# Kernel optimization log

Hardware: AMD Instinct MI355X
Metric: run time of the kernel (lower is better)

Reference implementation:

```python
import jax, jax.numpy as jnp
import numpy as np

B, S, D, H, DH, K, M = 2, 1024, 1024, 16, 64, 32, 8192
LN_EPS = 1e-5


def _ln(x, g, b):
    mu = jnp.mean(x, axis=-1, keepdims=True)
    var = jnp.var(x, axis=-1, keepdims=True)
    return (x - mu) * jax.lax.rsqrt(var + LN_EPS) * g + b


def _split_heads(t):  # [B,S,H*DH] -> [B,H,S,DH]
    return t.reshape(B, S, H, DH).transpose(0, 2, 1, 3)


def setup_inputs() -> dict:
    key = jax.random.key(0)
    ks = jax.random.split(key, 10)
    sd = 1.0 / np.sqrt(D)
    return {
        "x": jax.random.normal(ks[0], (B, S, D), jnp.float32),
        "mem_k_db": jax.random.normal(ks[1], (B, M, D), jnp.float32),
        "mem_v_db": jax.random.normal(ks[2], (B, M, D), jnp.float32),
        "g_val": jax.random.uniform(ks[3], (H,), jnp.float32),
        "ln1_g": jnp.ones((D,), jnp.float32),
        "ln1_b": jnp.zeros((D,), jnp.float32),
        "W_attn": jax.random.normal(ks[4], (D, 3 * D), jnp.float32) * sd,
        "b_attn": jnp.zeros((3 * D,), jnp.float32),
        "W_proj": jax.random.normal(ks[5], (D, D), jnp.float32) * sd,
        "b_proj": jnp.zeros((D,), jnp.float32),
        "ln2_g": jnp.ones((D,), jnp.float32),
        "ln2_b": jnp.zeros((D,), jnp.float32),
        "W_fc": jax.random.normal(ks[6], (D, 4 * D), jnp.float32) * sd,
        "b_fc": jnp.zeros((4 * D,), jnp.float32),
        "W_out": jax.random.normal(ks[7], (4 * D, D), jnp.float32) / np.sqrt(4 * D),
        "b_out": jnp.zeros((D,), jnp.float32),
    }


def reference(x, mem_k_db, mem_v_db, g_val, ln1_g, ln1_b, W_attn, b_attn,
              W_proj, b_proj, ln2_g, ln2_b, W_fc, b_fc, W_out, b_out):
    residual = x
    h = _ln(x, ln1_g, ln1_b)
    qkv = h @ W_attn + b_attn                       # [B,S,3D]
    q_f, k_f, v_f = jnp.split(qkv, 3, axis=-1)      # each [B,S,D]
    q = _split_heads(q_f)                           # [B,H,S,DH]
    k = _split_heads(k_f)
    v = _split_heads(v_f)

    # --- kNN memory search (non-per-head path): l2-normalized concat-head query ---
    sq = q_f / jnp.linalg.norm(q_f, axis=-1, keepdims=True).clip(1e-12)
    sims = jnp.einsum('bsd,bmd->bsm', sq, mem_k_db)          # [B,S,M]
    _, idx = jax.lax.top_k(sims, K)                          # [B,S,K]
    idx_e = idx[..., None]                                   # [B,S,K,1]
    mem_k = jnp.take_along_axis(mem_k_db[:, None], idx_e, axis=2)  # [B,S,K,D]
    mem_v = jnp.take_along_axis(mem_v_db[:, None], idx_e, axis=2)  # [B,S,K,D]
    # split memory into heads: [B,S,K,H*DH] -> [B,H,S,K,DH]
    mem_k = mem_k.reshape(B, S, K, H, DH).transpose(0, 3, 1, 2, 4)
    mem_v = mem_v.reshape(B, S, K, H, DH).transpose(0, 3, 1, 2, 4)

    inv_sqrt_dh = 1.0 / np.sqrt(DH)
    mem_w = jnp.einsum('bhid,bhijd->bhij', q, mem_k) * inv_sqrt_dh   # [B,H,S,K]

    std_w = jnp.einsum('bhid,bhjd->bhij', q, k) * inv_sqrt_dh        # [B,H,S,S]
    causal = jnp.tril(jnp.ones((S, S), bool))
    mask_val = jnp.finfo(std_w.dtype).min
    std_w = jnp.where(causal, std_w, mask_val)

    all_w = jax.nn.softmax(jnp.concatenate([mem_w, std_w], axis=-1), axis=-1)
    mem_attn, local_attn = all_w[..., :K], all_w[..., K:]

    local_out = jnp.einsum('bhij,bhjd->bhid', local_attn, v)
    mem_out = jnp.einsum('bhij,bhijd->bhid', mem_attn, mem_v)

    g = g_val.reshape(1, H, 1, 1)
    attn_out = (1.0 - g) * local_out + g * mem_out           # [B,H,S,DH]
    attn_out = attn_out.transpose(0, 2, 1, 3).reshape(B, S, D)
    attn_out = attn_out @ W_proj + b_proj

    h = attn_out + residual
    residual2 = h
    h = _ln(h, ln2_g, ln2_b)
    h = jax.nn.gelu(h @ W_fc + b_fc, approximate=True) @ W_out + b_out
    return residual2 + h
```

## Files before the change

kernel.cpp:

```cpp
#include <hip/hip_runtime.h>
#include <stdint.h>

#define DEV static __device__ __forceinline__

typedef __attribute__((ext_vector_type(8))) __bf16 bf16x8;
typedef __attribute__((ext_vector_type(4))) float f32x4;

DEV float bf2f(uint32_t u) {
  union { uint32_t i; float f; } v; v.i = u << 16; return v.f;
}
DEV uint16_t f2bf(float f) {
  union { float f; uint32_t i; } v; v.f = f;
  uint32_t x = v.i;
  return (uint16_t)((x + 0x7FFFu + ((x >> 16) & 1u)) >> 16);
}
DEV f32x4 mfma16(bf16x8 a, bf16x8 b, f32x4 c) {
  return __builtin_amdgcn_mfma_f32_16x16x32_bf16(a, b, c, 0, 0, 0);
}
DEV bf16x8 as_bf16x8(uint4 u) { return __builtin_bit_cast(bf16x8, u); }

DEV void gload16(const uint16_t* __restrict__ g, uint16_t* l) {
  __builtin_amdgcn_global_load_lds(
      (const __attribute__((address_space(1))) uint32_t*)g,
      (__attribute__((address_space(3))) uint32_t*)l, 16, 0, 0);
}

DEV float gelu_tanh(float x) {
  float x3 = x * x * x;
  float u = 0.7978845608028654f * (x + 0.044715f * x3);
  return 0.5f * x * (1.0f + tanhf(u));
}
DEV unsigned mono_key(float f) {
  union { float f; uint32_t u; } v; v.f = f;
  return (v.u & 0x80000000u) ? ~v.u : (v.u | 0x80000000u);
}
DEV unsigned mono16(unsigned u) {
  return (u & 0x8000u) ? (~u & 0xFFFFu) : (u | 0x8000u);
}

__global__ __launch_bounds__(256) void k_transpose_cast(
    const float* __restrict__ in, uint16_t* __restrict__ out,
    uint16_t* __restrict__ outlo, int R, int C) {
  __shared__ float tile[32][33];
  int c0 = blockIdx.x * 32, r0 = blockIdx.y * 32;
  int tx = threadIdx.x % 32, ty = threadIdx.x / 32;
  for (int i = 0; i < 32; i += 8)
    tile[ty + i][tx] = in[(size_t)(r0 + ty + i) * C + c0 + tx];
  __syncthreads();
  for (int i = 0; i < 32; i += 8) {
    float v = tile[tx][ty + i];
    uint16_t hi = f2bf(v);
    out[(size_t)(c0 + ty + i) * R + r0 + tx] = hi;
    if (outlo)
      outlo[(size_t)(c0 + ty + i) * R + r0 + tx] = f2bf(v - bf2f(hi));
  }
}

__global__ __launch_bounds__(256) void k_cast_bf16(
    const float* __restrict__ in, uint16_t* __restrict__ out, long n) {
  long i = ((long)blockIdx.x * 256 + threadIdx.x) * 4;
  if (i >= n) return;
  float4 v = *(const float4*)(in + i);
  uint2 pk;
  pk.x = (uint32_t)f2bf(v.x) | ((uint32_t)f2bf(v.y) << 16);
  pk.y = (uint32_t)f2bf(v.z) | ((uint32_t)f2bf(v.w) << 16);
  *(uint2*)(out + i) = pk;
}

__global__ __launch_bounds__(256) void k_layernorm(
    const float* __restrict__ x, const float* __restrict__ g,
    const float* __restrict__ bb, uint16_t* __restrict__ out,
    uint16_t* __restrict__ outlo) {
  int row = blockIdx.x;
  const float* xr = x + (size_t)row * 1024;
  int c = threadIdx.x * 4;
  float4 v = *(const float4*)(xr + c);
  float s = v.x + v.y + v.z + v.w;
  float s2 = v.x * v.x + v.y * v.y + v.z * v.z + v.w * v.w;
  for (int off = 32; off; off >>= 1) {
    s += __shfl_down(s, off, 64);
    s2 += __shfl_down(s2, off, 64);
  }
  __shared__ float ps[4], qs[4];
  int lane = threadIdx.x & 63, wv = threadIdx.x >> 6;
  if (!lane) { ps[wv] = s; qs[wv] = s2; }
  __syncthreads();
  float S = ps[0] + ps[1] + ps[2] + ps[3];
  float S2 = qs[0] + qs[1] + qs[2] + qs[3];
  float mu = S * (1.f / 1024.f);
  float var = S2 * (1.f / 1024.f) - mu * mu;
  float rinv = rsqrtf(var + 1e-5f);
  const float* vv = (const float*)&v;
  uint16_t o[4], ol[4];
#pragma unroll
  for (int j = 0; j < 4; j++) {
    float y = (vv[j] - mu) * rinv * g[c + j] + bb[c + j];
    o[j] = f2bf(y);
    ol[j] = f2bf(y - bf2f(o[j]));
  }
  uint2 pk;
  pk.x = (uint32_t)o[0] | ((uint32_t)o[1] << 16);
  pk.y = (uint32_t)o[2] | ((uint32_t)o[3] << 16);
  *(uint2*)(out + (size_t)row * 1024 + c) = pk;
  if (outlo) {
    pk.x = (uint32_t)ol[0] | ((uint32_t)ol[1] << 16);
    pk.y = (uint32_t)ol[2] | ((uint32_t)ol[3] << 16);
    *(uint2*)(outlo + (size_t)row * 1024 + c) = pk;
  }
}

template <int EPI>
__global__ __launch_bounds__(256) void k_gemm2(
    const uint16_t* __restrict__ A, int lda,
    const uint16_t* __restrict__ Bt, int ldb,
    void* __restrict__ Cout, int ldc,
    const float* __restrict__ bias,
    const float* __restrict__ resid,
    int Kc) {
  const int m0 = blockIdx.y * 64, n0 = blockIdx.x * 128;
  const int kt0 = (EPI & 16) ? blockIdx.z * Kc : 0;
  __shared__ __align__(16) uint16_t As[64 * 64];
  __shared__ __align__(16) uint16_t Bs[128 * 64];
  const int t = threadIdx.x, l = t & 63, w = t >> 6;
  const int lg = l >> 4, lr = l & 15;

  const int rS = t >> 3, cS = t & 7;
  const int csS = cS ^ (rS & 7);
  const uint16_t* pa1 = A + (size_t)(m0 + rS) * lda + kt0 + csS * 8;
  const uint16_t* pa2 = pa1 + (size_t)32 * lda;
  const uint16_t* pb1 = Bt + (size_t)(n0 + rS) * ldb + kt0 + csS * 8;
  const uint16_t* pb2 = pb1 + (size_t)32 * ldb;
  const uint16_t* pb3 = pb1 + (size_t)64 * ldb;
  const uint16_t* pb4 = pb1 + (size_t)96 * ldb;
  uint16_t* la1 = As + w * 512;
  uint16_t* la2 = As + 2048 + w * 512;
  uint16_t* lb1 = Bs + w * 512;
  uint16_t* lb2 = Bs + 2048 + w * 512;
  uint16_t* lb3 = Bs + 4096 + w * 512;
  uint16_t* lb4 = Bs + 6144 + w * 512;

  int offA[2][4], offB[2][2];
#pragma unroll
  for (int kk = 0; kk < 2; kk++) {
#pragma unroll
    for (int i = 0; i < 4; i++) {
      int row = i * 16 + lr;
      offA[kk][i] = row * 64 + (((kk * 4 + lg) ^ (row & 7)) * 8);
    }
#pragma unroll
    for (int j = 0; j < 2; j++) {
      int row = w * 32 + j * 16 + lr;
      offB[kk][j] = row * 64 + (((kk * 4 + lg) ^ (row & 7)) * 8);
    }
  }

  f32x4 acc[4][2] = {};
  for (int kt = 0; kt < Kc; kt += 64) {
    __syncthreads();
    gload16(pa1, la1); gload16(pa2, la2);
    gload16(pb1, lb1); gload16(pb2, lb2);
    gload16(pb3, lb3); gload16(pb4, lb4);
    pa1 += 64; pa2 += 64; pb1 += 64; pb2 += 64; pb3 += 64; pb4 += 64;
    __syncthreads();
#pragma unroll
    for (int kk = 0; kk < 2; kk++) {
      bf16x8 af[4], bfr[2];
#pragma unroll
      for (int i = 0; i < 4; i++) af[i] = as_bf16x8(*(const uint4*)(As + offA[kk][i]));
#pragma unroll
      for (int j = 0; j < 2; j++) bfr[j] = as_bf16x8(*(const uint4*)(Bs + offB[kk][j]));
#pragma unroll
      for (int i = 0; i < 4; i++)
#pragma unroll
        for (int j = 0; j < 2; j++)
          acc[i][j] = mfma16(af[i], bfr[j], acc[i][j]);
    }
  }
  const size_t zoff = (EPI & 16) ? (size_t)blockIdx.z * gridDim.y * 64 * ldc : 0;
#pragma unroll
  for (int i = 0; i < 4; i++)
#pragma unroll
    for (int j = 0; j < 2; j++)
#pragma unroll
      for (int r = 0; r < 4; r++) {
        int row = m0 + i * 16 + lg * 4 + r;
        int col = n0 + w * 32 + j * 16 + lr;
        float v = acc[i][j][r];
        if constexpr (EPI & 16) {
          ((float*)Cout)[zoff + (size_t)row * ldc + col] = v;
        } else {
          if constexpr (EPI & 1) v += bias[col];
          if constexpr (EPI & 4) v = gelu_tanh(v);
          if constexpr (EPI & 2) v += resid[(size_t)row * ldc + col];
          if constexpr (EPI & 8)
            ((uint16_t*)Cout)[(size_t)row * ldc + col] = f2bf(v);
          else
            ((float*)Cout)[(size_t)row * ldc + col] = v;
        }
      }
}

__global__ __launch_bounds__(256) void k_gemm_sims(
    const uint16_t* __restrict__ A,
    const uint16_t* __restrict__ Bt,
    uint16_t* __restrict__ Cout) {
  const int m0 = blockIdx.y * 64, n0 = blockIdx.x * 128;
  A += (size_t)blockIdx.z * 1024 * 3072;
  Bt += (size_t)blockIdx.z * 8192 * 1024;
  __shared__ __align__(16) uint16_t As[64 * 64];
  __shared__ __align__(16) uint16_t Bs[128 * 64];
  const int t = threadIdx.x, l = t & 63, w = t >> 6;
  const int lg = l >> 4, lr = l & 15;

  const int rS = t >> 3, cS = t & 7;
  const int csS = cS ^ (rS & 7);
  const uint16_t* pa1 = A + (size_t)(m0 + rS) * 3072 + csS * 8;
  const uint16_t* pa2 = pa1 + 32 * 3072;
  const uint16_t* pb1 = Bt + (size_t)(n0 + rS) * 1024 + csS * 8;
  const uint16_t* pb2 = pb1 + 32 * 1024;
  const uint16_t* pb3 = pb1 + 64 * 1024;
  const uint16_t* pb4 = pb1 + 96 * 1024;
  uint16_t* la1 = As + w * 512;
  uint16_t* la2 = As + 2048 + w * 512;
  uint16_t* lb1 = Bs + w * 512;
  uint16_t* lb2 = Bs + 2048 + w * 512;
  uint16_t* lb3 = Bs + 4096 + w * 512;
  uint16_t* lb4 = Bs + 6144 + w * 512;

  int offA[2][4], offB[2][2];
#pragma unroll
  for (int kk = 0; kk < 2; kk++) {
#pragma unroll
    for (int i = 0; i < 4; i++) {
      int row = i * 16 + lr;
      offA[kk][i] = row * 64 + (((kk * 4 + lg) ^ (row & 7)) * 8);
    }
#pragma unroll
    for (int j = 0; j < 2; j++) {
      int row = w * 32 + j * 16 + lr;
      offB[kk][j] = row * 64 + (((kk * 4 + lg) ^ (row & 7)) * 8);
    }
  }

  f32x4 acc[4][2] = {};
  for (int kt = 0; kt < 1024; kt += 64) {
    __syncthreads();
    gload16(pa1, la1); gload16(pa2, la2);
    gload16(pb1, lb1); gload16(pb2, lb2);
    gload16(pb3, lb3); gload16(pb4, lb4);
    pa1 += 64; pa2 += 64; pb1 += 64; pb2 += 64; pb3 += 64; pb4 += 64;
    __syncthreads();
#pragma unroll
    for (int kk = 0; kk < 2; kk++) {
      bf16x8 af[4], bfr[2];
#pragma unroll
      for (int i = 0; i < 4; i++) af[i] = as_bf16x8(*(const uint4*)(As + offA[kk][i]));
#pragma unroll
      for (int j = 0; j < 2; j++) bfr[j] = as_bf16x8(*(const uint4*)(Bs + offB[kk][j]));
#pragma unroll
      for (int i = 0; i < 4; i++)
#pragma unroll
        for (int j = 0; j < 2; j++)
          acc[i][j] = mfma16(af[i], bfr[j], acc[i][j]);
    }
  }
  const size_t zoff = (size_t)blockIdx.z * 1024 * 8192;
#pragma unroll
  for (int i = 0; i < 4; i++)
#pragma unroll
    for (int j = 0; j < 2; j++)
#pragma unroll
      for (int r = 0; r < 4; r++) {
        int row = m0 + i * 16 + lg * 4 + r;
        int col = n0 + w * 32 + j * 16 + lr;
        Cout[zoff + (size_t)row * 8192 + col] = f2bf(acc[i][j][r]);
      }
}

__global__ __launch_bounds__(256) void k_gemm_split2(
    const uint16_t* __restrict__ Ah, const uint16_t* __restrict__ Al, int lda,
    const uint16_t* __restrict__ Bh, const uint16_t* __restrict__ Bl, int ldb,
    uint16_t* __restrict__ Ch, uint16_t* __restrict__ Cl, int ldc,
    const float* __restrict__ bias, int Kd) {
  const int m0 = blockIdx.y * 64, n0 = blockIdx.x * 128;
  __shared__ __align__(16) uint16_t Ahs[64 * 64];
  __shared__ __align__(16) uint16_t Als[64 * 64];
  __shared__ __align__(16) uint16_t Bhs[128 * 64];
  __shared__ __align__(16) uint16_t Bls[128 * 64];
  const int t = threadIdx.x, l = t & 63, w = t >> 6;
  const int lg = l >> 4, lr = l & 15;

  const int rS = t >> 3, cS = t & 7;
  const int csS = cS ^ (rS & 7);
  const size_t ao1 = (size_t)(m0 + rS) * lda + csS * 8;
  const size_t bo1 = (size_t)(n0 + rS) * ldb + csS * 8;
  const uint16_t* pah1 = Ah + ao1; const uint16_t* pah2 = pah1 + (size_t)32 * lda;
  const uint16_t* pal1 = Al + ao1; const uint16_t* pal2 = pal1 + (size_t)32 * lda;
  const uint16_t* pbh1 = Bh + bo1; const uint16_t* pbh2 = pbh1 + (size_t)32 * ldb;
  const uint16_t* pbh3 = pbh1 + (size_t)64 * ldb; const uint16_t* pbh4 = pbh1 + (size_t)96 * ldb;
  const uint16_t* pbl1 = Bl + bo1; const uint16_t* pbl2 = pbl1 + (size_t)32 * ldb;
  const uint16_t* pbl3 = pbl1 + (size_t)64 * ldb; const uint16_t* pbl4 = pbl1 + (size_t)96 * ldb;
  uint16_t* lah1 = Ahs + w * 512; uint16_t* lah2 = Ahs + 2048 + w * 512;
  uint16_t* lal1 = Als + w * 512; uint16_t* lal2 = Als + 2048 + w * 512;
  uint16_t* lbh1 = Bhs + w * 512; uint16_t* lbh2 = Bhs + 2048 + w * 512;
  uint16_t* lbh3 = Bhs + 4096 + w * 512; uint16_t* lbh4 = Bhs + 6144 + w * 512;
  uint16_t* lbl1 = Bls + w * 512; uint16_t* lbl2 = Bls + 2048 + w * 512;
  uint16_t* lbl3 = Bls + 4096 + w * 512; uint16_t* lbl4 = Bls + 6144 + w * 512;

  int offA[2][4], offB[2][2];
#pragma unroll
  for (int kk = 0; kk < 2; kk++) {
#pragma unroll
    for (int i = 0; i < 4; i++) {
      int row = i * 16 + lr;
      offA[kk][i] = row * 64 + (((kk * 4 + lg) ^ (row & 7)) * 8);
    }
#pragma unroll
    for (int j = 0; j < 2; j++) {
      int row = w * 32 + j * 16 + lr;
      offB[kk][j] = row * 64 + (((kk * 4 + lg) ^ (row & 7)) * 8);
    }
  }

  f32x4 acc[4][2] = {};
  for (int kt = 0; kt < Kd; kt += 64) {
    __syncthreads();
    gload16(pah1, lah1); gload16(pah2, lah2);
    gload16(pal1, lal1); gload16(pal2, lal2);
    gload16(pbh1, lbh1); gload16(pbh2, lbh2);
    gload16(pbh3, lbh3); gload16(pbh4, lbh4);
    gload16(pbl1, lbl1); gload16(pbl2, lbl2);
    gload16(pbl3, lbl3); gload16(pbl4, lbl4);
    pah1 += 64; pah2 += 64; pal1 += 64; pal2 += 64;
    pbh1 += 64; pbh2 += 64; pbh3 += 64; pbh4 += 64;
    pbl1 += 64; pbl2 += 64; pbl3 += 64; pbl4 += 64;
    __syncthreads();
#pragma unroll
    for (int kk = 0; kk < 2; kk++) {
      bf16x8 ah[4], al[4], bh[2], bl[2];
#pragma unroll
      for (int i = 0; i < 4; i++) {
        ah[i] = as_bf16x8(*(const uint4*)(Ahs + offA[kk][i]));
        al[i] = as_bf16x8(*(const uint4*)(Als + offA[kk][i]));
      }
#pragma unroll
      for (int j = 0; j < 2; j++) {
        bh[j] = as_bf16x8(*(const uint4*)(Bhs + offB[kk][j]));
        bl[j] = as_bf16x8(*(const uint4*)(Bls + offB[kk][j]));
      }
#pragma unroll
      for (int i = 0; i < 4; i++)
#pragma unroll
        for (int j = 0; j < 2; j++) {
          acc[i][j] = mfma16(ah[i], bh[j], acc[i][j]);
          acc[i][j] = mfma16(ah[i], bl[j], acc[i][j]);
          acc[i][j] = mfma16(al[i], bh[j], acc[i][j]);
        }
    }
  }
#pragma unroll
  for (int i = 0; i < 4; i++)
#pragma unroll
    for (int j = 0; j < 2; j++)
#pragma unroll
      for (int r = 0; r < 4; r++) {
        int row = m0 + i * 16 + lg * 4 + r;
        int col = n0 + w * 32 + j * 16 + lr;
        float v = acc[i][j][r] + bias[col];
        uint16_t hi = f2bf(v);
        Ch[(size_t)row * ldc + col] = hi;
        Cl[(size_t)row * ldc + col] = f2bf(v - bf2f(hi));
      }
}

template <int NP>
__global__ __launch_bounds__(256) void k_merge(
    const float* __restrict__ parts, const float* __restrict__ bias,
    const float* __restrict__ resid, float* __restrict__ out) {
  int row = blockIdx.x, c = threadIdx.x * 4;
  size_t off = (size_t)row * 1024 + c;
  float4 s = *(const float4*)(resid + off);
  float4 bv = *(const float4*)(bias + c);
  s.x += bv.x; s.y += bv.y; s.z += bv.z; s.w += bv.w;
#pragma unroll
  for (int z = 0; z < NP; z++) {
    float4 pv = *(const float4*)(parts + (size_t)z * 2048 * 1024 + off);
    s.x += pv.x; s.y += pv.y; s.z += pv.z; s.w += pv.w;
  }
  *(float4*)(out + off) = s;
}

__global__ __launch_bounds__(256) void k_topk2(
    const uint16_t* __restrict__ simsb,
    const uint16_t* __restrict__ qkvh_b,
    const uint16_t* __restrict__ qkvl_b,
    const float* __restrict__ memk_b,
    int* __restrict__ idx_out,
    float* __restrict__ mlogh) {
  int grow = blockIdx.x;
  int z = grow >> 10;
  int t = threadIdx.x;
  const uint16_t* s16 = simsb + (size_t)grow * 8192;
  const float* memk = memk_b + (size_t)z * 8192 * 1024;
  unsigned key[32];
#pragma unroll
  for (int k = 0; k < 4; k++) {
    uint4 u = *(const uint4*)(s16 + t * 8 + k * 2048);
    const uint16_t* pu = (const uint16_t*)&u;
#pragma unroll
    for (int j = 0; j < 8; j++) key[k * 8 + j] = mono16(pu[j]);
  }
  __shared__ int partial[2][4];
  __shared__ int cnt_s;
  __shared__ int sidx[40];
  __shared__ float qs[1024];
  __shared__ float hval[40][16];
  int lane = t & 63, wv = t >> 6;
  unsigned lo = 0u, hi = 0xFFFFu;
  for (int it = 0; it < 16; ++it) {
    unsigned mid = lo + ((hi - lo) >> 1);
    int c = 0;
#pragma unroll
    for (int i = 0; i < 32; i++) c += (key[i] > mid) ? 1 : 0;
    for (int off = 32; off; off >>= 1) c += __shfl_down(c, off, 64);
    if (!lane) partial[it & 1][wv] = c;
    __syncthreads();
    int tot = partial[it & 1][0] + partial[it & 1][1] +
              partial[it & 1][2] + partial[it & 1][3];
    if (tot >= 40) lo = mid + 1; else hi = mid;
  }
  unsigned T = lo;
  if (t == 0) cnt_s = 0;
  __syncthreads();
#pragma unroll
  for (int i = 0; i < 32; i++)
    if (key[i] > T) {
      int p = atomicAdd(&cnt_s, 1);
      if (p < 40) sidx[p] = t * 8 + (i >> 3) * 2048 + (i & 7);
    }
  __syncthreads();
#pragma unroll
  for (int i = 0; i < 32; i++)
    if (key[i] == T) {
      int p = atomicAdd(&cnt_s, 1);
      if (p < 40) sidx[p] = t * 8 + (i >> 3) * 2048 + (i & 7);
    }
  {
    int c4 = t * 4;
    const uint16_t* qh = qkvh_b + (size_t)grow * 3072;
    const uint16_t* ql = qkvl_b + (size_t)grow * 3072;
    uint2 uh = *(const uint2*)(qh + c4);
    uint2 ul = *(const uint2*)(ql + c4);
    qs[c4 + 0] = bf2f(uh.x & 0xFFFF) + bf2f(ul.x & 0xFFFF);
    qs[c4 + 1] = bf2f(uh.x >> 16) + bf2f(ul.x >> 16);
    qs[c4 + 2] = bf2f(uh.y & 0xFFFF) + bf2f(ul.y & 0xFFFF);
    qs[c4 + 3] = bf2f(uh.y >> 16) + bf2f(ul.y >> 16);
  }
  __syncthreads();
  {
    float4 qreg[4];
#pragma unroll
    for (int i = 0; i < 4; i++) qreg[i] = *(const float4*)(qs + i * 256 + lane * 4);
    for (int cc = 0; cc < 10; ++cc) {
      int c = wv * 10 + cc;
      const float* kp = memk + (size_t)sidx[c] * 1024;
#pragma unroll
      for (int i = 0; i < 4; ++i) {
        float4 kv = *(const float4*)(kp + i * 256 + lane * 4);
        float pband = kv.x * qreg[i].x + kv.y * qreg[i].y +
                      kv.z * qreg[i].z + kv.w * qreg[i].w;
        pband += __shfl_xor(pband, 1, 64);
        pband += __shfl_xor(pband, 2, 64);
        pband += __shfl_xor(pband, 4, 64);
        pband += __shfl_xor(pband, 8, 64);
        if ((lane & 15) == 0) hval[c][i * 4 + (lane >> 4)] = pband;
      }
    }
  }
  __syncthreads();
  if (wv == 0) {
    float full = 0.f;
    if (t < 40) {
#pragma unroll
      for (int i = 0; i < 16; i++) full += hval[t][i];
    }
    unsigned k2 = (t < 40) ? mono_key(full) : 0u;
    unsigned lo2 = 0u, hi2 = 0xFFFFFFFFu;
    for (int it = 0; it < 32; ++it) {
      unsigned mid = lo2 + ((hi2 - lo2) >> 1);
      int c = __popcll(__ballot(k2 > mid));
      if (c >= 32) lo2 = mid + 1; else hi2 = mid;
    }
    unsigned T2 = lo2;
    unsigned long long m1 = __ballot(k2 > T2);
    unsigned long long m2 = __ballot(k2 == T2);
    int n1 = __popcll(m1);
    unsigned long long lt = ((unsigned long long)1 << t) - 1;
    int pos = 99;
    if (k2 > T2) pos = __popcll(m1 & lt);
    else if (k2 == T2 && t < 40) pos = n1 + __popcll(m2 & lt);
    if (pos < 32) {
      idx_out[(size_t)grow * 32 + pos] = sidx[t];
#pragma unroll
      for (int i = 0; i < 16; i++)
        mlogh[((size_t)grow * 32 + pos) * 16 + i] = hval[t][i] * 0.125f;
    }
  }
}

__global__ __launch_bounds__(256) void k_flash(
    const uint16_t* __restrict__ qkvh,
    const uint16_t* __restrict__ qkvl,
    float* __restrict__ pacc,
    float* __restrict__ pm,
    float* __restrict__ pl) {
  const int qt = blockIdx.x, chk = blockIdx.y, bh = blockIdx.z;
  const int cbase = chk * 256;
  if (cbase >= (qt + 1) * 64) return;
  const int b = bh >> 4, h = bh & 15;
  const int t = threadIdx.x, lane = t & 63, w = t >> 6;
  const int lg = lane >> 4, lr = lane & 15;
  const int q0 = qt * 64 + w * 16;
  const size_t rowb = (size_t)b * 1024;
  __shared__ __align__(16) uint16_t Kh[2048];
  __shared__ __align__(16) uint16_t Kl[2048];
  __shared__ __align__(16) uint16_t Vs[2048];
  __shared__ __align__(16) uint16_t Pl[4][16][40];

  bf16x8 qh[2], qlo[2];
  {
    const uint16_t* qph = qkvh + (rowb + q0 + lr) * 3072 + h * 64;
    const uint16_t* qpl = qkvl + (rowb + q0 + lr) * 3072 + h * 64;
    qh[0] = as_bf16x8(*(const uint4*)(qph + lg * 8));
    qh[1] = as_bf16x8(*(const uint4*)(qph + 32 + lg * 8));
    qlo[0] = as_bf16x8(*(const uint4*)(qpl + lg * 8));
    qlo[1] = as_bf16x8(*(const uint4*)(qpl + 32 + lg * 8));
  }
  f32x4 acc[4] = {};
  float mrow[4], lrowv[4];
#pragma unroll
  for (int r = 0; r < 4; r++) { mrow[r] = -1e30f; lrowv[r] = 0.f; }

  const int lim = min(cbase + 256, q0 + 16);
  const int blim = min(cbase + 256, (qt + 1) * 64);

  const int sr = t >> 3, sc = t & 7;
  const int scs = sc ^ (sr & 7);
  const uint16_t* gkh = qkvh + (rowb + sr) * 3072 + 1024 + h * 64 + scs * 8;
  const uint16_t* gkl = qkvl + (rowb + sr) * 3072 + 1024 + h * 64 + scs * 8;
  const uint16_t* gv  = qkvh + (rowb + sr) * 3072 + 2048 + h * 64 + scs * 8;
  uint16_t* lkh = Kh + w * 512;
  uint16_t* lkl = Kl + w * 512;
  uint16_t* lv  = Vs + w * 512;

  for (int c0 = cbase; c0 < blim; c0 += 32) {
    const size_t so = (size_t)c0 * 3072;
    gload16(gkh + so, lkh);
    gload16(gkl + so, lkl);
    gload16(gv + so, lv);
    __syncthreads();
    if (c0 < lim) {
      f32x4 sf[2];
#pragma unroll
      for (int n = 0; n < 2; n++) {
        const int row = n * 16 + lr;
        const int rb = row * 64;
        const int x0 = ((lg) ^ (row & 7)) * 8;
        const int x1 = ((4 + lg) ^ (row & 7)) * 8;
        bf16x8 kh0 = as_bf16x8(*(const uint4*)(Kh + rb + x0));
        bf16x8 kh1 = as_bf16x8(*(const uint4*)(Kh + rb + x1));
        bf16x8 kl0 = as_bf16x8(*(const uint4*)(Kl + rb + x0));
        bf16x8 kl1 = as_bf16x8(*(const uint4*)(Kl + rb + x1));
        f32x4 sz = {};
        sz = mfma16(qh[0], kh0, sz);
        sz = mfma16(qh[1], kh1, sz);
        sz = mfma16(qh[0], kl0, sz);
        sz = mfma16(qh[1], kl1, sz);
        sz = mfma16(qlo[0], kh0, sz);
        sz = mfma16(qlo[1], kh1, sz);
        sf[n] = sz;
      }
      float p0[4], p1[4], alpha[4];
#pragma unroll
      for (int r = 0; r < 4; r++) {
        int rowq = q0 + lg * 4 + r;
        int col0 = c0 + lr, col1 = c0 + 16 + lr;
        float s0 = sf[0][r] * 0.125f; if (col0 > rowq) s0 = -1e30f;
        float s1 = sf[1][r] * 0.125f; if (col1 > rowq) s1 = -1e30f;
        float mt = fmaxf(s0, s1);
        mt = fmaxf(mt, __shfl_xor(mt, 1, 64));
        mt = fmaxf(mt, __shfl_xor(mt, 2, 64));
        mt = fmaxf(mt, __shfl_xor(mt, 4, 64));
        mt = fmaxf(mt, __shfl_xor(mt, 8, 64));
        float mnew = fmaxf(mrow[r], mt);
        float a = __expf(mrow[r] - mnew);
        float e0 = __expf(s0 - mnew), e1 = __expf(s1 - mnew);
        float ss = e0 + e1;
        ss += __shfl_xor(ss, 1, 64);
        ss += __shfl_xor(ss, 2, 64);
        ss += __shfl_xor(ss, 4, 64);
        ss += __shfl_xor(ss, 8, 64);
        lrowv[r] = lrowv[r] * a + ss;
        mrow[r] = mnew;
        alpha[r] = a;
        p0[r] = e0; p1[r] = e1;
      }
#pragma unroll
      for (int nv = 0; nv < 4; nv++)
#pragma unroll
        for (int r = 0; r < 4; r++) acc[nv][r] *= alpha[r];
#pragma unroll
      for (int r = 0; r < 4; r++) {
        Pl[w][lg * 4 + r][lr] = f2bf(p0[r]);
        Pl[w][lg * 4 + r][16 + lr] = f2bf(p1[r]);
      }
      bf16x8 pa = as_bf16x8(*(const uint4*)&Pl[w][lr][lg * 8]);
#pragma unroll
      for (int nv = 0; nv < 4; nv++) {
        const int col = nv * 16 + lr;
        const int cc = col >> 3, cl = col & 7;
        uint32_t vv[8];
#pragma unroll
        for (int j = 0; j < 8; j++) {
          int row = lg * 8 + j;
          vv[j] = Vs[row * 64 + ((cc ^ (row & 7)) * 8 + cl)];
        }
        uint4 pk;
        pk.x = vv[0] | (vv[1] << 16);
        pk.y = vv[2] | (vv[3] << 16);
        pk.z = vv[4] | (vv[5] << 16);
        pk.w = vv[6] | (vv[7] << 16);
        acc[nv] = mfma16(pa, as_bf16x8(pk), acc[nv]);
      }
    }
    __syncthreads();
  }
  const size_t base = (size_t)(chk * 32 + bh) * 1024;
#pragma unroll
  for (int nv = 0; nv < 4; nv++)
#pragma unroll
    for (int r = 0; r < 4; r++) {
      int rowq = q0 + lg * 4 + r;
      pacc[(base + rowq) * 64 + nv * 16 + lr] = acc[nv][r];
    }
  if (lr == 0) {
#pragma unroll
    for (int r = 0; r < 4; r++) {
      int rowq = q0 + lg * 4 + r;
      pm[base + rowq] = mrow[r];
      pl[base + rowq] = lrowv[r];
    }
  }
}

__global__ __launch_bounds__(256) void k_memcombine(
    const float* __restrict__ mlogh,
    const float* __restrict__ memv,
    const int* __restrict__ idx,
    const float* __restrict__ pacc,
    const float* __restrict__ pm,
    const float* __restrict__ pl,
    const float* __restrict__ gval,
    uint16_t* __restrict__ attnout) {
  int row = blockIdx.x;
  int b = row >> 10, s = row & 1023;
  int qt = s >> 6;
  int nact = (qt >> 2) + 1;
  __shared__ int sidx[32];
  __shared__ float lg[16][32];
  __shared__ float sp[16][32];
  __shared__ float smx[16], ssum[16];
  __shared__ float scl[16][4], Ms[16], Ls[16];
  int t = threadIdx.x;
  if (t < 32) sidx[t] = idx[(size_t)row * 32 + t];
  {
    const float* mp = mlogh + (size_t)row * 512;
#pragma unroll
    for (int rep = 0; rep < 2; rep++) {
      int i = t + rep * 256;
      lg[i & 15][i >> 4] = mp[i];
    }
  }
  __syncthreads();
  if (t < 16) {
    float mx = -1e30f;
#pragma unroll
    for (int j = 0; j < 32; j++) mx = fmaxf(mx, lg[t][j]);
    float su = 0.f;
    for (int j = 0; j < 32; j++) {
      float e = __expf(lg[t][j] - mx);
      sp[t][j] = e; su += e;
    }
    smx[t] = mx; ssum[t] = su;
  } else if (t >= 64 && t < 80) {
    int hh = t - 64;
    float pmv[4];
    float M = -1e30f;
    for (int c = 0; c < nact; c++) {
      pmv[c] = pm[(size_t)(c * 32 + b * 16 + hh) * 1024 + s];
      M = fmaxf(M, pmv[c]);
    }
    float L = 0.f;
    for (int c = 0; c < nact; c++) {
      float e = __expf(pmv[c] - M);
      scl[hh][c] = e;
      L += e * pl[(size_t)(c * 32 + b * 16 + hh) * 1024 + s];
    }
    Ms[hh] = M; Ls[hh] = L;
  }
  __syncthreads();
#pragma unroll
  for (int cc = 0; cc < 4; cc++) {
    int col = t + cc * 256;
    int hh = col >> 6;
    float ma = 0.f;
#pragma unroll
    for (int j = 0; j < 32; j++)
      ma += sp[hh][j] * memv[((size_t)b * 8192 + sidx[j]) * 1024 + col];
    float la = 0.f;
    for (int c = 0; c < nact; c++)
      la += scl[hh][c] *
            pacc[((size_t)(c * 32 + b * 16 + hh) * 1024 + s) * 64 + (col & 63)];
    float ms = Ms[hh], ls = Ls[hh];
    float mm = smx[hh], lmm = ssum[hh];
    float Mx = fmaxf(ms, mm);
    float es = __expf(ms - Mx), em = __expf(mm - Mx);
    float L = es * ls + em * lmm;
    float gh = gval[hh];
    float o = ((1.f - gh) * es * la + gh * em * ma) / L;
    attnout[(size_t)row * 1024 + col] = f2bf(o);
  }
}

extern "C" void kernel_launch(void* const* d_in, const int* in_sizes, int n_in,
                              void* d_out, int out_size, void* d_ws, size_t ws_size,
                              hipStream_t stream) {
  (void)in_sizes; (void)n_in; (void)out_size; (void)ws_size;
  const float* x     = (const float*)d_in[0];
  const float* memkf = (const float*)d_in[1];
  const float* memvf = (const float*)d_in[2];
  const float* gval  = (const float*)d_in[3];
  const float* ln1g  = (const float*)d_in[4];
  const float* ln1b  = (const float*)d_in[5];
  const float* Wattn = (const float*)d_in[6];
  const float* battn = (const float*)d_in[7];
  const float* Wproj = (const float*)d_in[8];
  const float* bproj = (const float*)d_in[9];
  const float* ln2g  = (const float*)d_in[10];
  const float* ln2b  = (const float*)d_in[11];
  const float* Wfc   = (const float*)d_in[12];
  const float* bfc   = (const float*)d_in[13];
  const float* Wout  = (const float*)d_in[14];
  const float* bout  = (const float*)d_in[15];

  char* p = (char*)d_ws;
  auto alloc = [&](size_t bytes) -> char* {
    char* r = p;
    p += (bytes + 255) & ~(size_t)255;
    return r;
  };
  uint16_t* h_hi    = (uint16_t*)alloc(2048ull * 1024 * 2);
  uint16_t* h_lo    = (uint16_t*)alloc(2048ull * 1024 * 2);
  uint16_t* WattnTh = (uint16_t*)alloc(3072ull * 1024 * 2);
  uint16_t* WattnTl = (uint16_t*)alloc(3072ull * 1024 * 2);
  uint16_t* WprojT  = (uint16_t*)alloc(1024ull * 1024 * 2);
  uint16_t* WfcT    = (uint16_t*)alloc(4096ull * 1024 * 2);
  uint16_t* WoutT   = (uint16_t*)alloc(1024ull * 4096 * 2);
  uint16_t* memk_bf = (uint16_t*)alloc(2ull * 8192 * 1024 * 2);
  uint16_t* qkv_hi  = (uint16_t*)alloc(2048ull * 3072 * 2);
  uint16_t* qkv_lo  = (uint16_t*)alloc(2048ull * 3072 * 2);
  float*    sims    = (float*)alloc(1024ull * 8192 * 4);
  int*      idx     = (int*)alloc(2048ull * 32 * 4);
  float*    mlogh   = (float*)alloc(2048ull * 32 * 16 * 4);
  float*    pm      = (float*)alloc(4ull * 32 * 1024 * 4);
  float*    pl      = (float*)alloc(4ull * 32 * 1024 * 4);
  float*    h1      = (float*)alloc(2048ull * 1024 * 4);
  uint16_t* attn_bf = (uint16_t*)alloc(2048ull * 1024 * 2);
  uint16_t* h2_bf   = h_hi;
  uint16_t* simsb   = (uint16_t*)sims;
  float*    pacc    = sims;
  uint16_t* ffn1    = (uint16_t*)sims;
  float*    parts   = (float*)memk_bf;

  k_transpose_cast<<<dim3(96, 32), 256, 0, stream>>>(Wattn, WattnTh, WattnTl, 1024, 3072);
  k_transpose_cast<<<dim3(32, 32), 256, 0, stream>>>(Wproj, WprojT, nullptr, 1024, 1024);
  k_transpose_cast<<<dim3(128, 32), 256, 0, stream>>>(Wfc, WfcT, nullptr, 1024, 4096);
  k_transpose_cast<<<dim3(32, 128), 256, 0, stream>>>(Wout, WoutT, nullptr, 4096, 1024);
  k_cast_bf16<<<16384, 256, 0, stream>>>(memkf, memk_bf, 2l * 8192 * 1024);

  k_layernorm<<<2048, 256, 0, stream>>>(x, ln1g, ln1b, h_hi, h_lo);
  k_gemm_split2<<<dim3(24, 32), 256, 0, stream>>>(h_hi, h_lo, 1024, WattnTh, WattnTl, 1024,
                                                  qkv_hi, qkv_lo, 3072, battn, 1024);
  k_gemm_sims<<<dim3(64, 16, 2), 256, 0, stream>>>(qkv_hi, memk_bf, simsb);
  k_topk2<<<2048, 256, 0, stream>>>(simsb, qkv_hi, qkv_lo, memkf, idx, mlogh);
  k_flash<<<dim3(16, 4, 32), 256, 0, stream>>>(qkv_hi, qkv_lo, pacc, pm, pl);
  k_memcombine<<<2048, 256, 0, stream>>>(mlogh, memvf, idx, pacc, pm, pl, gval, attn_bf);
  k_gemm2<16><<<dim3(8, 32, 2), 256, 0, stream>>>(attn_bf, 1024, WprojT, 1024,
                                                  parts, 1024, nullptr, nullptr, 512);
  k_merge<2><<<2048, 256, 0, stream>>>(parts, bproj, x, h1);
  k_layernorm<<<2048, 256, 0, stream>>>(h1, ln2g, ln2b, h2_bf, nullptr);
  k_gemm2<13><<<dim3(32, 32), 256, 0, stream>>>(h2_bf, 1024, WfcT, 1024,
                                                ffn1, 4096, bfc, nullptr, 1024);
  k_gemm2<16><<<dim3(8, 32, 4), 256, 0, stream>>>(ffn1, 4096, WoutT, 4096,
                                                  parts, 1024, nullptr, nullptr, 1024);
  k_merge<4><<<2048, 256, 0, stream>>>(parts, bout, h1, (float*)d_out);
}
```

Before: 396.5 us.

## Fuse top-k and flash attention into one launch sharing dynamic block ranges

```diff
diff --git a/kernel.cpp b/kernel.cpp
--- a/kernel.cpp
+++ b/kernel.cpp
@@ -390,18 +390,24 @@
   *(float4*)(out + off) = s;
 }
 
-__global__ __launch_bounds__(256) void k_topk2(
+
+DEV void topk2_body(
+    char* smem, int grow,
     const uint16_t* __restrict__ simsb,
     const uint16_t* __restrict__ qkvh_b,
     const uint16_t* __restrict__ qkvl_b,
     const float* __restrict__ memk_b,
     int* __restrict__ idx_out,
     float* __restrict__ mlogh) {
-  int grow = blockIdx.x;
   int z = grow >> 10;
   int t = threadIdx.x;
   const uint16_t* s16 = simsb + (size_t)grow * 8192;
   const float* memk = memk_b + (size_t)z * 8192 * 1024;
+  int* partial = (int*)smem;
+  int* cnt_s = (int*)(smem + 32);
+  int* sidx = (int*)(smem + 64);
+  float* qs = (float*)(smem + 256);
+  float* hval = (float*)(smem + 4352);
   unsigned key[32];
 #pragma unroll
   for (int k = 0; k < 4; k++) {
@@ -410,11 +416,6 @@
 #pragma unroll
     for (int j = 0; j < 8; j++) key[k * 8 + j] = mono16(pu[j]);
   }
-  __shared__ int partial[2][4];
-  __shared__ int cnt_s;
-  __shared__ int sidx[40];
-  __shared__ float qs[1024];
-  __shared__ float hval[40][16];
   int lane = t & 63, wv = t >> 6;
   unsigned lo = 0u, hi = 0xFFFFu;
   for (int it = 0; it < 16; ++it) {
@@ -423,26 +424,26 @@
 #pragma unroll
     for (int i = 0; i < 32; i++) c += (key[i] > mid) ? 1 : 0;
     for (int off = 32; off; off >>= 1) c += __shfl_down(c, off, 64);
-    if (!lane) partial[it & 1][wv] = c;
+    if (!lane) partial[(it & 1) * 4 + wv] = c;
     __syncthreads();
-    int tot = partial[it & 1][0] + partial[it & 1][1] +
-              partial[it & 1][2] + partial[it & 1][3];
+    int tot = partial[(it & 1) * 4 + 0] + partial[(it & 1) * 4 + 1] +
+              partial[(it & 1) * 4 + 2] + partial[(it & 1) * 4 + 3];
     if (tot >= 40) lo = mid + 1; else hi = mid;
   }
   unsigned T = lo;
-  if (t == 0) cnt_s = 0;
+  if (t == 0) *cnt_s = 0;
   __syncthreads();
 #pragma unroll
   for (int i = 0; i < 32; i++)
     if (key[i] > T) {
-      int p = atomicAdd(&cnt_s, 1);
+      int p = atomicAdd(cnt_s, 1);
       if (p < 40) sidx[p] = t * 8 + (i >> 3) * 2048 + (i & 7);
     }
   __syncthreads();
 #pragma unroll
   for (int i = 0; i < 32; i++)
     if (key[i] == T) {
-      int p = atomicAdd(&cnt_s, 1);
+      int p = atomicAdd(cnt_s, 1);
       if (p < 40) sidx[p] = t * 8 + (i >> 3) * 2048 + (i & 7);
     }
   {
@@ -473,7 +474,7 @@
         pband += __shfl_xor(pband, 2, 64);
         pband += __shfl_xor(pband, 4, 64);
         pband += __shfl_xor(pband, 8, 64);
-        if ((lane & 15) == 0) hval[c][i * 4 + (lane >> 4)] = pband;
+        if ((lane & 15) == 0) hval[c * 16 + i * 4 + (lane >> 4)] = pband;
       }
     }
   }
@@ -482,7 +483,7 @@
     float full = 0.f;
     if (t < 40) {
 #pragma unroll
-      for (int i = 0; i < 16; i++) full += hval[t][i];
+      for (int i = 0; i < 16; i++) full += hval[t * 16 + i];
     }
     unsigned k2 = (t < 40) ? mono_key(full) : 0u;
     unsigned lo2 = 0u, hi2 = 0xFFFFFFFFu;
@@ -503,18 +504,19 @@
       idx_out[(size_t)grow * 32 + pos] = sidx[t];
 #pragma unroll
       for (int i = 0; i < 16; i++)
-        mlogh[((size_t)grow * 32 + pos) * 16 + i] = hval[t][i] * 0.125f;
-    }
-  }
-}
-
-__global__ __launch_bounds__(256) void k_flash(
+        mlogh[((size_t)grow * 32 + pos) * 16 + i] = hval[t * 16 + i] * 0.125f;
+    }
+  }
+}
+
+DEV void flash_body(
+    char* smem, int id,
     const uint16_t* __restrict__ qkvh,
     const uint16_t* __restrict__ qkvl,
     float* __restrict__ pacc,
     float* __restrict__ pm,
     float* __restrict__ pl) {
-  const int qt = blockIdx.x, chk = blockIdx.y, bh = blockIdx.z;
+  const int qt = id & 15, chk = (id >> 4) & 3, bh = id >> 6;
   const int cbase = chk * 256;
   if (cbase >= (qt + 1) * 64) return;
   const int b = bh >> 4, h = bh & 15;
@@ -522,10 +524,10 @@
   const int lg = lane >> 4, lr = lane & 15;
   const int q0 = qt * 64 + w * 16;
   const size_t rowb = (size_t)b * 1024;
-  __shared__ __align__(16) uint16_t Kh[2048];
-  __shared__ __align__(16) uint16_t Kl[2048];
-  __shared__ __align__(16) uint16_t Vs[2048];
-  __shared__ __align__(16) uint16_t Pl[4][16][40];
+  uint16_t* Kh = (uint16_t*)smem;
+  uint16_t* Kl = (uint16_t*)(smem + 4096);
+  uint16_t* Vs = (uint16_t*)(smem + 8192);
+  uint16_t* Pl = (uint16_t*)(smem + 12288);
 
   bf16x8 qh[2], qlo[2];
   {
@@ -611,10 +613,10 @@
         for (int r = 0; r < 4; r++) acc[nv][r] *= alpha[r];
 #pragma unroll
       for (int r = 0; r < 4; r++) {
-        Pl[w][lg * 4 + r][lr] = f2bf(p0[r]);
-        Pl[w][lg * 4 + r][16 + lr] = f2bf(p1[r]);
-      }
-      bf16x8 pa = as_bf16x8(*(const uint4*)&Pl[w][lr][lg * 8]);
+        Pl[(w * 16 + lg * 4 + r) * 40 + lr] = f2bf(p0[r]);
+        Pl[(w * 16 + lg * 4 + r) * 40 + 16 + lr] = f2bf(p1[r]);
+      }
+      bf16x8 pa = as_bf16x8(*(const uint4*)&Pl[(w * 16 + lr) * 40 + lg * 8]);
 #pragma unroll
       for (int nv = 0; nv < 4; nv++) {
         const int col = nv * 16 + lr;
@@ -651,6 +653,23 @@
       pl[base + rowq] = lrowv[r];
     }
   }
+}
+
+__global__ __launch_bounds__(256) void k_fused(
+    const uint16_t* __restrict__ simsb,
+    const uint16_t* __restrict__ qkvh,
+    const uint16_t* __restrict__ qkvl,
+    const float* __restrict__ memk_b,
+    int* __restrict__ idx_out,
+    float* __restrict__ mlogh,
+    float* __restrict__ pacc,
+    float* __restrict__ pm,
+    float* __restrict__ pl) {
+  __shared__ __align__(16) char smem[17536];
+  if (blockIdx.x < 2048)
+    topk2_body(smem, blockIdx.x, simsb, qkvh, qkvl, memk_b, idx_out, mlogh);
+  else
+    flash_body(smem, blockIdx.x - 2048, qkvh, qkvl, pacc, pm, pl);
 }
 
 __global__ __launch_bounds__(256) void k_memcombine(
@@ -778,7 +797,7 @@
   uint16_t* attn_bf = (uint16_t*)alloc(2048ull * 1024 * 2);
   uint16_t* h2_bf   = h_hi;
   uint16_t* simsb   = (uint16_t*)sims;
-  float*    pacc    = sims;
+  float*    pacc    = (float*)memk_bf;
   uint16_t* ffn1    = (uint16_t*)sims;
   float*    parts   = (float*)memk_bf;
 
@@ -792,8 +811,7 @@
   k_gemm_split2<<<dim3(24, 32), 256, 0, stream>>>(h_hi, h_lo, 1024, WattnTh, WattnTl, 1024,
                                                   qkv_hi, qkv_lo, 3072, battn, 1024);
   k_gemm_sims<<<dim3(64, 16, 2), 256, 0, stream>>>(qkv_hi, memk_bf, simsb);
-  k_topk2<<<2048, 256, 0, stream>>>(simsb, qkv_hi, qkv_lo, memkf, idx, mlogh);
-  k_flash<<<dim3(16, 4, 32), 256, 0, stream>>>(qkv_hi, qkv_lo, pacc, pm, pl);
+  k_fused<<<4096, 256, 0, stream>>>(simsb, qkv_hi, qkv_lo, memkf, idx, mlogh, pacc, pm, pl);
   k_memcombine<<<2048, 256, 0, stream>>>(mlogh, memvf, idx, pacc, pm, pl, gval, attn_bf);
   k_gemm2<16><<<dim3(8, 32, 2), 256, 0, stream>>>(attn_bf, 1024, WprojT, 1024,
                                                   parts, 1024, nullptr, nullptr, 512);
```

Result: no change. 402.1 us (+1.4%).
